# Optimization experiments

Measured on AMD Instinct MI355X. Metric: run time of the kernel, lower is better.

The kernel has to match this reference:

```python
import jax, jax.numpy as jnp
import numpy as np

B, L, C = 2, 1024, 512
H, P = 8, 4
D = C // H
LN_EPS = 1e-5


def setup_inputs() -> dict:
    key = jax.random.key(0)
    ks = jax.random.split(key, 12)
    s = 0.02
    inp = {
        "features": jax.random.normal(ks[0], (B, L, C), jnp.float32),
        "coords": jax.random.normal(ks[1], (B, L, 3), jnp.float32),
        # LayerNorm params
        "ln_g": jnp.ones((C,), jnp.float32),
        "ln_b": jnp.zeros((C,), jnp.float32),
        # scalar q/k/v projections (stored as [in, out])
        "wq": jax.random.normal(ks[2], (C, C), jnp.float32) * s,
        "bq": jnp.zeros((C,), jnp.float32),
        "wk": jax.random.normal(ks[3], (C, C), jnp.float32) * s,
        "bk": jnp.zeros((C,), jnp.float32),
        "wv": jax.random.normal(ks[4], (C, C), jnp.float32) * s,
        "bv": jnp.zeros((C,), jnp.float32),
        # point q/k/v projections: [C, H*P*3]
        "wqp": jax.random.normal(ks[5], (C, H * P * 3), jnp.float32) * s,
        "bqp": jnp.zeros((H * P * 3,), jnp.float32),
        "wkp": jax.random.normal(ks[6], (C, H * P * 3), jnp.float32) * s,
        "bkp": jnp.zeros((H * P * 3,), jnp.float32),
        "wvp": jax.random.normal(ks[7], (C, H * P * 3), jnp.float32) * s,
        "bvp": jnp.zeros((H * P * 3,), jnp.float32),
        # output projection
        "wo": jax.random.normal(ks[8], (C, C), jnp.float32) * s,
        "bo": jnp.zeros((C,), jnp.float32),
        # per-head point scale, init 1/sqrt(P)
        "pscale": jnp.full((H,), 1.0 / np.sqrt(P), jnp.float32),
    }
    return inp


def _layernorm(x, g, b):
    mu = jnp.mean(x, axis=-1, keepdims=True)
    var = jnp.mean((x - mu) ** 2, axis=-1, keepdims=True)
    return (x - mu) * jax.lax.rsqrt(var + LN_EPS) * g + b


def reference(features, coords, ln_g, ln_b, wq, bq, wk, bk, wv, bv,
              wqp, bqp, wkp, bkp, wvp, bvp, wo, bo, pscale):
    b, l, c = features.shape
    h = pscale.shape[0]
    d = c // h
    p = wqp.shape[1] // (h * 3)

    x = _layernorm(features, ln_g, ln_b)

    # scalar heads: [b,h,l,d]
    q_s = (x @ wq + bq).reshape(b, l, h, d).transpose(0, 2, 1, 3)
    k_s = (x @ wk + bk).reshape(b, l, h, d).transpose(0, 2, 1, 3)
    v_s = (x @ wv + bv).reshape(b, l, h, d).transpose(0, 2, 1, 3)

    # point heads: [b,h,l,p,3]
    q_p = (x @ wqp + bqp).reshape(b, l, h, p, 3).transpose(0, 2, 1, 3, 4)
    k_p = (x @ wkp + bkp).reshape(b, l, h, p, 3).transpose(0, 2, 1, 3, 4)

    # scalar logits
    logits_s = jnp.einsum('bhid,bhjd->bhij', q_s, k_s) * (d ** -0.5)

    # point-distance logits: sum_{p,k} ||q - k||^2 = |q|^2 + |k|^2 - 2 q.k
    # (avoids materializing the [b,h,l,l,p,3] difference tensor)
    dot = jnp.einsum('bhipk,bhjpk->bhij', q_p, k_p)
    qsq = jnp.sum(q_p * q_p, axis=(-1, -2))  # [b,h,l]
    ksq = jnp.sum(k_p * k_p, axis=(-1, -2))  # [b,h,l]
    pdist2 = qsq[..., :, None] + ksq[..., None, :] - 2.0 * dot  # [b,h,l,l]

    logits = logits_s - pdist2 * pscale[None, :, None, None]

    attn = jax.nn.softmax(logits, axis=-1)  # dropout is identity in eval

    out_s = jnp.einsum('bhij,bhjd->bhid', attn, v_s)
    out_s = out_s.transpose(0, 2, 1, 3).reshape(b, l, c)

    out = out_s @ wo + bo  # out_dropout is identity in eval
    return out
```

## Files before the change

kernel.cpp:

```cpp
#include <hip/hip_runtime.h>
#include <math.h>

#define BB 2
#define LL 1024
#define CCH 512
#define HH 8
#define LN_EPSF 1e-5f

typedef short s16x8 __attribute__((ext_vector_type(8)));
typedef float fx4 __attribute__((ext_vector_type(4)));


__device__ __forceinline__ unsigned short f2bf(float f) {
  unsigned u = __float_as_uint(f);
  unsigned r = (u + 0x7FFFu + ((u >> 16) & 1u)) >> 16;
  return (unsigned short)r;
}
__device__ __forceinline__ float bf2f(unsigned short h) {
  return __uint_as_float(((unsigned)h) << 16);
}
__device__ __forceinline__ s16x8 ldfrag(const unsigned short* p) {
  int4 t = *(const int4*)p;
  return *(s16x8*)&t;
}

template <int CTRL>
__device__ __forceinline__ float dpp_mov(float x) {
  return __int_as_float(
      __builtin_amdgcn_update_dpp(0, __float_as_int(x), CTRL, 0xF, 0xF, true));
}
__device__ __forceinline__ float red16_sum(float v) {
  v += dpp_mov<0x121>(v);
  v += dpp_mov<0x122>(v);
  v += dpp_mov<0x124>(v);
  v += dpp_mov<0x128>(v);
  return v;
}
__device__ __forceinline__ float red16_max(float v) {
  v = fmaxf(v, dpp_mov<0x121>(v));
  v = fmaxf(v, dpp_mov<0x122>(v));
  v = fmaxf(v, dpp_mov<0x124>(v));
  v = fmaxf(v, dpp_mov<0x128>(v));
  return v;
}
__device__ __forceinline__ float wave_sum(float v) {
  v = red16_sum(v);
  v += __shfl_xor(v, 16);
  v += __shfl_xor(v, 32);
  return v;
}

__global__ __launch_bounds__(256) void prep(
    const float* __restrict__ f, const float* __restrict__ g,
    const float* __restrict__ bta, unsigned short* __restrict__ xh,
    unsigned short* __restrict__ xl, const float* __restrict__ wq,
    const float* __restrict__ wk, const float* __restrict__ wv,
    const float* __restrict__ wo, const float* __restrict__ wqp,
    const float* __restrict__ wkp, unsigned short* __restrict__ wt_h) {
  __shared__ unsigned short lh[64][68];
  __shared__ float red[8];
  const int tid = threadIdx.x;
  if (blockIdx.x < 2048) {
    const int row = blockIdx.x;
    const int wave = tid >> 6, lane = tid & 63;
    const float* fr = f + (size_t)row * CCH;
    float2 v = *(const float2*)&fr[tid * 2];
    float s = wave_sum(v.x + v.y);
    if (lane == 0) red[wave] = s;
    __syncthreads();
    float mu = (red[0] + red[1] + red[2] + red[3]) * (1.0f / CCH);
    float dx = v.x - mu, dy = v.y - mu;
    float sq = wave_sum(dx * dx + dy * dy);
    if (lane == 0) red[4 + wave] = sq;
    __syncthreads();
    float var = (red[4] + red[5] + red[6] + red[7]) * (1.0f / CCH);
    float inv = 1.0f / sqrtf(var + LN_EPSF);
    float2 gg = *(const float2*)&g[tid * 2];
    float2 bb = *(const float2*)&bta[tid * 2];
    float ox = dx * inv * gg.x + bb.x;
    float oy = dy * inv * gg.y + bb.y;
    unsigned short h0 = f2bf(ox), h1 = f2bf(oy);
    ushort2 hv; hv.x = h0; hv.y = h1;
    ushort2 lv; lv.x = f2bf(ox - bf2f(h0)); lv.y = f2bf(oy - bf2f(h1));
    const int k0c = tid * 2;
    size_t addr = ((size_t)((row >> 4) * 16 + (k0c >> 5))) * 512 +
                  (((k0c >> 3) & 3) * 16 + (row & 15)) * 8 + (k0c & 7);
    *(ushort2*)&xh[addr] = hv;
    *(ushort2*)&xl[addr] = lv;
  } else {
    const int bx = blockIdx.x - 2048;
    const float* W;
    int Ncols, rowbase, kt, nt;
    if (bx < 256) {
      int mat = bx >> 6, t = bx & 63;
      kt = t >> 3; nt = t & 7; Ncols = 512;
      if (mat == 0) { W = wq; rowbase = 0; }
      else if (mat == 1) { W = wk; rowbase = 512; }
      else if (mat == 2) { W = wv; rowbase = 1024; }
      else { W = wo; rowbase = 1536; }
    } else {
      int r = bx - 256; int mat = r >> 4; int t = r & 15;
      kt = t >> 1; nt = t & 1; Ncols = 96;
      if (mat == 0) { W = wqp; rowbase = 2048; }
      else { W = wkp; rowbase = 2144; }
    }
    const int k0 = kt * 64, n0 = nt * 64;
    const int c = tid & 63;
#pragma unroll
    for (int ii = 0; ii < 16; ++ii) {
      int r = ii * 4 + (tid >> 6);
      float val = (n0 + c < Ncols) ? W[(size_t)(k0 + r) * Ncols + n0 + c] : 0.f;
      lh[r][c] = f2bf(val);
    }
    __syncthreads();
    const int base_nt = (rowbase >> 4) + (n0 >> 4);
    const int base_kt = (k0 >> 5);
#pragma unroll
    for (int cc = 0; cc < 2; ++cc) {
      int ch = cc * 256 + tid;
      int lane2 = ch & 63, ktl = (ch >> 6) & 1, ntl = ch >> 7;
      int l16c = lane2 & 15, quadc = lane2 >> 4;
      if (n0 + ntl * 16 < Ncols) {
        unsigned short th[8] __attribute__((aligned(16)));
#pragma unroll
        for (int jj = 0; jj < 8; ++jj)
          th[jj] = lh[ktl * 32 + quadc * 8 + jj][ntl * 16 + l16c];
        *(int4*)&wt_h[((size_t)((base_nt + ntl) * 16 + base_kt + ktl)) * 512 +
                      lane2 * 8] = *(int4*)th;
      }
    }
  }
}

template <int MF, int NF, int TERMS>
__device__ __forceinline__ void mfma_core_frag(
    const unsigned short* __restrict__ Ah, const unsigned short* __restrict__ Al,
    const unsigned short* __restrict__ Bt, int mt0, int ntbase, int nt0,
    int ntmax, int ks0, int ks1, fx4 acc[MF][NF]) {
  const int lane = threadIdx.x & 63;
  int bt[NF];
#pragma unroll
  for (int j = 0; j < NF; ++j) {
    int nt = nt0 + j;
    if (nt > ntmax) nt = ntmax;
    bt[j] = ntbase + nt;
  }
#pragma unroll
  for (int i = 0; i < MF; ++i)
#pragma unroll
    for (int j = 0; j < NF; ++j) acc[i][j] = (fx4){0.f, 0.f, 0.f, 0.f};
  for (int ks = ks0; ks < ks1; ++ks) {
    s16x8 ah[MF], al[MF], b[NF];
#pragma unroll
    for (int i = 0; i < MF; ++i) {
      size_t off = ((size_t)((mt0 + i) * 16 + ks)) * 512 + lane * 8;
      ah[i] = ldfrag(&Ah[off]);
      if (TERMS == 2) al[i] = ldfrag(&Al[off]);
    }
#pragma unroll
    for (int j = 0; j < NF; ++j)
      b[j] = ldfrag(&Bt[((size_t)(bt[j] * 16 + ks)) * 512 + lane * 8]);
#pragma unroll
    for (int i = 0; i < MF; ++i)
#pragma unroll
      for (int j = 0; j < NF; ++j) {
        acc[i][j] = __builtin_amdgcn_mfma_f32_16x16x32_bf16(ah[i], b[j], acc[i][j], 0, 0, 0);
        if (TERMS == 2)
          acc[i][j] = __builtin_amdgcn_mfma_f32_16x16x32_bf16(al[i], b[j], acc[i][j], 0, 0, 0);
      }
  }
}

__global__ __launch_bounds__(256, 4) void proj_mfma(
    const unsigned short* __restrict__ xh, const unsigned short* __restrict__ xl,
    const unsigned short* __restrict__ wt_h,
    const float* __restrict__ bq, const float* __restrict__ bk,
    const float* __restrict__ bv, const float* __restrict__ bqp,
    const float* __restrict__ bkp, const float* __restrict__ pscale,
    unsigned short* __restrict__ qt, unsigned short* __restrict__ kt_,
    unsigned short* __restrict__ vth) {
  __shared__ unsigned short vt_lds[64][72];
  const int bx = blockIdx.x;
  const int m0 = blockIdx.y * 64;
  const int tid = threadIdx.x;
  const int wave = __builtin_amdgcn_readfirstlane(tid >> 6);
  const int lane = tid & 63;
  const int quad = lane >> 4, l16 = lane & 15;
  const int mw = m0 + (wave & 1) * 32;
  const int mt0 = mw >> 4;

  if (bx < 16) {
    const bool isq = bx < 8;
    const float* bias = isq ? bq : bk;
    unsigned short* pdst = isq ? qt : kt_;
    const int n0 = (bx & 7) * 64;
    const int nw = n0 + (wave >> 1) * 32;
    fx4 acc[2][2];
    mfma_core_frag<2, 2, 1>(xh, xh, wt_h, mt0, isq ? 0 : 32, nw >> 4, 31, 0, 16, acc);
#pragma unroll
    for (int j = 0; j < 2; ++j) {
      int n = nw + j * 16 + l16;
      int h = n >> 6, d = n & 63;
      float bb = bias[n];
#pragma unroll
      for (int i = 0; i < 2; ++i)
#pragma unroll
        for (int reg = 0; reg < 4; ++reg) {
          int row = mw + i * 16 + quad * 4 + reg;
          int bi = row >> 10, l = row & 1023;
          int bh2 = bi * 8 + h;
          float val = (acc[i][j][reg] + bb) * 0.35355339059f;
          size_t tile = ((size_t)(bh2 * 64 + (l >> 4))) * 3 + (d >> 5);
          pdst[tile * 512 + (((d >> 3) & 3) * 16 + (l & 15)) * 8 + (d & 7)] = f2bf(val);
        }
    }
  } else if (bx < 24) {
    const int h = bx - 16;
    const int nw = h * 64 + (wave >> 1) * 32;
    fx4 acc[2][2];
    mfma_core_frag<2, 2, 2>(xh, xl, wt_h, mt0, 64, nw >> 4, 31, 0, 16, acc);
#pragma unroll
    for (int j = 0; j < 2; ++j) {
      int dl = (wave >> 1) * 32 + j * 16 + l16;
      float bb = bv[h * 64 + dl];
#pragma unroll
      for (int i = 0; i < 2; ++i)
#pragma unroll
        for (int reg = 0; reg < 4; ++reg) {
          int lm = (wave & 1) * 32 + i * 16 + quad * 4 + reg;
          vt_lds[lm][dl] = f2bf(acc[i][j][reg] + bb);
        }
    }
    __syncthreads();
    const int b = m0 >> 10, l0 = m0 & 1023;
    const int bh2 = b * 8 + h;
#pragma unroll
    for (int cc = 0; cc < 2; ++cc) {
      int ch = cc * 256 + tid;
      int lane2 = ch & 63, jt = (ch >> 6) & 1, ft = ch >> 7;
      int l16c = lane2 & 15, quadc = lane2 >> 4;
      unsigned short th[8] __attribute__((aligned(16)));
#pragma unroll
      for (int jj = 0; jj < 8; ++jj)
        th[jj] = vt_lds[jt * 32 + quadc * 8 + jj][ft * 16 + l16c];
      size_t tile = ((size_t)(bh2 * 4 + ft)) * 32 + (l0 >> 5) + jt;
      *(int4*)&vth[tile * 512 + lane2 * 8] = *(int4*)th;
    }
  } else {
    const bool isq = bx < 26;
    const float* bias = isq ? bqp : bkp;
    unsigned short* pdst = isq ? qt : kt_;
    const int n0 = (bx & 1) * 64;
    const int nw = n0 + (wave >> 1) * 32;
    fx4 acc[2][2];
    mfma_core_frag<2, 2, 1>(xh, xh, wt_h, mt0, isq ? 128 : 134, nw >> 4, 5, 0, 16, acc);
#pragma unroll
    for (int j = 0; j < 2; ++j) {
      int n = nw + j * 16 + l16;
      bool ok = n < 96;
      int nn = ok ? n : 0;
      int h = nn / 12, c = nn - h * 12;
      float sc = sqrtf(2.f * pscale[h]);
      float bb = bias[nn];
#pragma unroll
      for (int i = 0; i < 2; ++i)
#pragma unroll
        for (int reg = 0; reg < 4; ++reg) {
          int row = mw + i * 16 + quad * 4 + reg;
          int bi = row >> 10, l = row & 1023;
          int bh2 = bi * 8 + h;
          float val = (acc[i][j][reg] + bb) * sc;
          if (ok) {
            int kc = 64 + c;
            size_t tile = ((size_t)(bh2 * 64 + (l >> 4))) * 3 + 2;
            pdst[tile * 512 + (((kc >> 3) & 3) * 16 + (l & 15)) * 8 + (kc & 7)] =
                f2bf(val);
          }
        }
    }
  }
}

__global__ __launch_bounds__(256, 4) void out_proj_mfma(
    const unsigned short* __restrict__ oh,
    const unsigned short* __restrict__ wt_h, const float* __restrict__ bo,
    float* __restrict__ out) {
  const int tid = threadIdx.x;
  const int wave = __builtin_amdgcn_readfirstlane(tid >> 6);
  const int lane = tid & 63;
  const int quad = lane >> 4, l16 = lane & 15;
  const int mw = blockIdx.y * 64 + (wave & 1) * 32;
  const int nw = blockIdx.x * 64 + (wave >> 1) * 32;
  const int kz = blockIdx.z;
  fx4 acc[2][2];
  mfma_core_frag<2, 2, 1>(oh, oh, wt_h, mw >> 4, 96, nw >> 4, 31, kz * 4,
                          kz * 4 + 4, acc);
#pragma unroll
  for (int j = 0; j < 2; ++j) {
    int n = nw + j * 16 + l16;
    float bb = (kz == 0) ? bo[n] : 0.f;
#pragma unroll
    for (int i = 0; i < 2; ++i)
#pragma unroll
      for (int reg = 0; reg < 4; ++reg) {
        int row = mw + i * 16 + quad * 4 + reg;
        atomicAdd(&out[(size_t)row * 512 + n], acc[i][j][reg] + bb);
      }
  }
}

__global__ __launch_bounds__(256, 4) void ipa_attn_mfma(
    const unsigned short* __restrict__ qt, const unsigned short* __restrict__ kt_,
    const unsigned short* __restrict__ vth,
    float* __restrict__ po, float* __restrict__ pm, float* __restrict__ pl) {
  const int bid = blockIdx.x;
  const int low3 = bid & 7;
  const int slot = bid >> 3;
  const int qtile = slot & 31;
  const int t = slot >> 5;
  const int ksz = t & 1;
  const int bh = ((t >> 1) << 3) | low3;
  const int tid = threadIdx.x;
  const int wave = tid >> 6, lane = tid & 63;
  const int quad = lane >> 4, l16 = lane & 15;
  const int mstrip = wave & 1, khalf = wave >> 1;
  const int ibase = qtile * 32 + mstrip * 16;

  __shared__ unsigned short pb[4][16][32];
  __shared__ float obuf[4][16][64];
  __shared__ float mred[4][16], lred[4][16];
  __shared__ float qsl[4][16];

  s16x8 aq[3];
#pragma unroll
  for (int s = 0; s < 3; ++s)
    aq[s] = ldfrag(&qt[(((size_t)(bh * 64 + (ibase >> 4))) * 3 + s) * 512 + lane * 8]);

  {
    float qp = 0.f;
#pragma unroll
    for (int j = 0; j < 8; ++j) {
      float v = bf2f((unsigned short)aq[2][j]);
      qp += v * v;
    }
    qp += __shfl_xor(qp, 16);
    qp += __shfl_xor(qp, 32);
    qsl[wave][l16] = 0.5f * qp;
  }
  float qs_r[4];
#pragma unroll
  for (int reg = 0; reg < 4; ++reg) qs_r[reg] = qsl[wave][quad * 4 + reg];

  fx4 o[4];
#pragma unroll
  for (int f = 0; f < 4; ++f) o[f] = (fx4){0.f, 0.f, 0.f, 0.f};
  float m_r[4], l_r[4];
#pragma unroll
  for (int reg = 0; reg < 4; ++reg) { m_r[reg] = -INFINITY; l_r[reg] = 0.f; }

  for (int kt2 = ksz * 8; kt2 < ksz * 8 + 8; ++kt2) {
    const int j0 = kt2 * 64 + khalf * 32;
    s16x8 bk[2][3];
#pragma unroll
    for (int f = 0; f < 2; ++f)
#pragma unroll
      for (int s = 0; s < 3; ++s)
        bk[f][s] = ldfrag(
            &kt_[(((size_t)(bh * 64 + (j0 >> 4) + f)) * 3 + s) * 512 + lane * 8]);
    s16x8 bvh[4];
#pragma unroll
    for (int f = 0; f < 4; ++f)
      bvh[f] = ldfrag(
          &vth[(((size_t)(bh * 4 + f)) * 32 + (j0 >> 5)) * 512 + lane * 8]);

    float kp0 = 0.f, kp1 = 0.f;
#pragma unroll
    for (int j = 0; j < 8; ++j) {
      float v0 = bf2f((unsigned short)bk[0][2][j]);
      float v1 = bf2f((unsigned short)bk[1][2][j]);
      kp0 += v0 * v0;
      kp1 += v1 * v1;
    }
    kp0 += __shfl_xor(kp0, 16);
    kp0 += __shfl_xor(kp0, 32);
    kp1 += __shfl_xor(kp1, 16);
    kp1 += __shfl_xor(kp1, 32);
    float ks0 = 0.5f * kp0, ks1 = 0.5f * kp1;

    fx4 sa[2];
    sa[0] = (fx4){0.f, 0.f, 0.f, 0.f};
    sa[1] = (fx4){0.f, 0.f, 0.f, 0.f};
#pragma unroll
    for (int f = 0; f < 2; ++f)
#pragma unroll
      for (int s = 0; s < 3; ++s)
        sa[f] = __builtin_amdgcn_mfma_f32_16x16x32_bf16(aq[s], bk[f][s], sa[f], 0, 0, 0);

#pragma unroll
    for (int reg = 0; reg < 4; ++reg) {
      float z0 = sa[0][reg] - qs_r[reg] - ks0;
      float z1 = sa[1][reg] - qs_r[reg] - ks1;
      float mx = red16_max(fmaxf(z0, z1));
      float mnew = fmaxf(m_r[reg], mx);
      float p0 = __expf(z0 - mnew), p1 = __expf(z1 - mnew);
      float alpha = __expf(m_r[reg] - mnew);
      float psum = red16_sum(p0 + p1);
      l_r[reg] = l_r[reg] * alpha + psum;
      m_r[reg] = mnew;
      o[0][reg] *= alpha; o[1][reg] *= alpha; o[2][reg] *= alpha; o[3][reg] *= alpha;
      pb[wave][quad * 4 + reg][l16] = f2bf(p0);
      pb[wave][quad * 4 + reg][16 + l16] = f2bf(p1);
    }
    s16x8 ap = ldfrag(&pb[wave][l16][quad * 8]);
#pragma unroll
    for (int f = 0; f < 4; ++f)
      o[f] = __builtin_amdgcn_mfma_f32_16x16x32_bf16(ap, bvh[f], o[f], 0, 0, 0);
  }
  if (l16 == 0) {
#pragma unroll
    for (int reg = 0; reg < 4; ++reg) {
      mred[wave][quad * 4 + reg] = m_r[reg];
      lred[wave][quad * 4 + reg] = l_r[reg];
    }
  }
#pragma unroll
  for (int f = 0; f < 4; ++f)
#pragma unroll
    for (int reg = 0; reg < 4; ++reg)
      obuf[wave][quad * 4 + reg][f * 16 + l16] = o[f][reg];
  __syncthreads();
  if (khalf == 0) {
    const int pw = wave + 2;
    const size_t rbase = ((size_t)ksz * 16 + bh) * LL + ibase;
#pragma unroll
    for (int f = 0; f < 4; ++f)
#pragma unroll
      for (int reg = 0; reg < 4; ++reg) {
        int row = quad * 4 + reg;
        int d = f * 16 + l16;
        float m0v = mred[wave][row], m1v = mred[pw][row];
        float l0v = lred[wave][row], l1v = lred[pw][row];
        float M = fmaxf(m0v, m1v);
        float w0 = __expf(m0v - M), w1 = __expf(m1v - M);
        float Lv = l0v * w0 + l1v * w1;
        float val = obuf[wave][row][d] * w0 + obuf[pw][row][d] * w1;
        po[(rbase + row) * 64 + d] = val;
        if (f == 0 && l16 == 0) {
          pm[rbase + row] = M;
          pl[rbase + row] = Lv;
        }
      }
  }
}

__global__ __launch_bounds__(256) void merge_attn(const float* __restrict__ po,
                                                  const float* __restrict__ pm,
                                                  const float* __restrict__ pl,
                                                  unsigned short* __restrict__ oh) {
  const int r = blockIdx.x * 4 + (threadIdx.x >> 6);
  const int lane = threadIdx.x & 63;
  const size_t part = (size_t)16 * LL;
  float m0 = pm[r], m1 = pm[part + r];
  float l0 = pl[r], l1 = pl[part + r];
  float M = fmaxf(m0, m1);
  float w0 = __expf(m0 - M), w1 = __expf(m1 - M);
  float L = l0 * w0 + l1 * w1;
  float v = (po[(size_t)r * 64 + lane] * w0 + po[(part + r) * 64 + lane] * w1) / L;
  int bh = r >> 10, l = r & 1023;
  int b = bh >> 3, h = bh & 7;
  int m = b * LL + l;
  int kcol = h * 64 + lane;
  size_t tile = ((size_t)(m >> 4)) * 16 + (kcol >> 5);
  oh[tile * 512 + (((kcol >> 3) & 3) * 16 + (m & 15)) * 8 + (kcol & 7)] = f2bf(v);
}

extern "C" void kernel_launch(void* const* d_in, const int* in_sizes, int n_in,
                              void* d_out, int out_size, void* d_ws, size_t ws_size,
                              hipStream_t stream) {
  (void)in_sizes; (void)n_in; (void)out_size; (void)ws_size;
  const float* features = (const float*)d_in[0];
  const float* ln_g = (const float*)d_in[2];
  const float* ln_b = (const float*)d_in[3];
  const float* wq = (const float*)d_in[4];
  const float* bq = (const float*)d_in[5];
  const float* wk = (const float*)d_in[6];
  const float* bk = (const float*)d_in[7];
  const float* wv = (const float*)d_in[8];
  const float* bv = (const float*)d_in[9];
  const float* wqp = (const float*)d_in[10];
  const float* bqp = (const float*)d_in[11];
  const float* wkp = (const float*)d_in[12];
  const float* bkp = (const float*)d_in[13];
  const float* wo = (const float*)d_in[16];
  const float* bo = (const float*)d_in[17];
  const float* pscale = (const float*)d_in[18];
  float* out = (float*)d_out;

  char* cur = (char*)d_ws;
  const size_t NTOK = (size_t)BB * LL;
  unsigned short* xh = (unsigned short*)cur; cur += NTOK * CCH * 2;
  unsigned short* xl = (unsigned short*)cur; cur += NTOK * CCH * 2;
  unsigned short* wt_h = (unsigned short*)cur; cur += (size_t)2240 * 512 * 2;
  unsigned short* qt = (unsigned short*)cur; cur += (size_t)16 * LL * 96 * 2;
  unsigned short* kt_ = (unsigned short*)cur; cur += (size_t)16 * LL * 96 * 2;
  unsigned short* vth = (unsigned short*)cur; cur += (size_t)16 * 64 * LL * 2;
  unsigned short* oh = (unsigned short*)cur; cur += NTOK * CCH * 2;
  float* po = (float*)cur; cur += (size_t)2 * 16 * LL * 64 * 4;
  float* pm = (float*)cur; cur += (size_t)2 * 16 * LL * 4;
  float* pl = (float*)cur; cur += (size_t)2 * 16 * LL * 4;

  hipMemsetAsync(qt, 0, (size_t)2 * 16 * LL * 96 * 2, stream);
  hipMemsetAsync(out, 0, NTOK * CCH * 4, stream);

  prep<<<dim3(2048 + 288), 256, 0, stream>>>(features, ln_g, ln_b, xh, xl, wq, wk,
                                             wv, wo, wqp, wkp, wt_h);
  proj_mfma<<<dim3(28, 32), 256, 0, stream>>>(xh, xl, wt_h, bq, bk, bv, bqp, bkp,
                                              pscale, qt, kt_, vth);
  ipa_attn_mfma<<<dim3(1024), 256, 0, stream>>>(qt, kt_, vth, po, pm, pl);
  merge_attn<<<dim3(4096), 256, 0, stream>>>(po, pm, pl, oh);
  out_proj_mfma<<<dim3(8, 32, 4), 256, 0, stream>>>(oh, wt_h, bo, out);
}
```

Before: 165.8 us.

## Fuse split-K merge into attention kernel and fold memsets into prep

The attention kernel now uses 512-thread blocks with four key-quarter waves per query strip, so the full key range is processed in one block and the softmax partials are combined in shared memory before writing bf16 output directly. This removes the separate merge_attn kernel and the fp32 partial-output round trip through global memory. The two hipMemsetAsync calls are replaced by extra prep blocks that zero only the needed padding region of qt/kt and the output buffer, which cuts launches. In exchange there are half as many attention blocks, each with a larger shared-memory footprint, so occupancy and parallelism drop.

```diff
diff --git a/kernel.cpp b/kernel.cpp
--- a/kernel.cpp
+++ b/kernel.cpp
@@ -56,12 +56,15 @@
     unsigned short* __restrict__ xl, const float* __restrict__ wq,
     const float* __restrict__ wk, const float* __restrict__ wv,
     const float* __restrict__ wo, const float* __restrict__ wqp,
-    const float* __restrict__ wkp, unsigned short* __restrict__ wt_h) {
+    const float* __restrict__ wkp, unsigned short* __restrict__ wt_h,
+    unsigned short* __restrict__ qt, unsigned short* __restrict__ kt_,
+    float* __restrict__ out) {
   __shared__ unsigned short lh[64][68];
   __shared__ float red[8];
   const int tid = threadIdx.x;
-  if (blockIdx.x < 2048) {
-    const int row = blockIdx.x;
+  const int bxg = blockIdx.x;
+  if (bxg < 2048) {
+    const int row = bxg;
     const int wave = tid >> 6, lane = tid & 63;
     const float* fr = f + (size_t)row * CCH;
     float2 v = *(const float2*)&fr[tid * 2];
@@ -87,8 +90,8 @@
                   (((k0c >> 3) & 3) * 16 + (row & 15)) * 8 + (k0c & 7);
     *(ushort2*)&xh[addr] = hv;
     *(ushort2*)&xl[addr] = lv;
-  } else {
-    const int bx = blockIdx.x - 2048;
+  } else if (bxg < 2336) {
+    const int bx = bxg - 2048;
     const float* W;
     int Ncols, rowbase, kt, nt;
     if (bx < 256) {
@@ -129,6 +132,24 @@
                       lane2 * 8] = *(int4*)th;
       }
     }
+  } else if (bxg < 2400) {
+    const int vb2 = bxg - 2336;
+    const int4 zero = {0, 0, 0, 0};
+    for (int u = tid; u < 32 * 48; u += 256) {
+      int t = u / 48, off = (u - t * 48) * 8;
+      int gidx = vb2 * 32 + t;
+      unsigned short* dst = (gidx < 1024) ? qt : kt_;
+      int rem = gidx & 1023;
+      int bh = rem >> 6, lt = rem & 63;
+      size_t base = ((size_t)(bh * 64 + lt) * 3 + 2) * 512;
+      *(int4*)&dst[base + 128 + off] = zero;
+    }
+  } else {
+    const int vb3 = bxg - 2400;
+    const float4 zero = {0.f, 0.f, 0.f, 0.f};
+    float4* dst = (float4*)(out + (size_t)vb3 * 4096);
+#pragma unroll
+    for (int i = 0; i < 4; ++i) dst[i * 256 + tid] = zero;
   }
 }
 
@@ -309,27 +330,24 @@
   }
 }
 
-__global__ __launch_bounds__(256, 4) void ipa_attn_mfma(
+__global__ __launch_bounds__(512, 4) void ipa_attn_mfma(
     const unsigned short* __restrict__ qt, const unsigned short* __restrict__ kt_,
-    const unsigned short* __restrict__ vth,
-    float* __restrict__ po, float* __restrict__ pm, float* __restrict__ pl) {
+    const unsigned short* __restrict__ vth, unsigned short* __restrict__ oh) {
   const int bid = blockIdx.x;
   const int low3 = bid & 7;
   const int slot = bid >> 3;
   const int qtile = slot & 31;
-  const int t = slot >> 5;
-  const int ksz = t & 1;
-  const int bh = ((t >> 1) << 3) | low3;
+  const int bh = ((slot >> 5) << 3) | low3;
   const int tid = threadIdx.x;
   const int wave = tid >> 6, lane = tid & 63;
   const int quad = lane >> 4, l16 = lane & 15;
-  const int mstrip = wave & 1, khalf = wave >> 1;
+  const int mstrip = wave & 1, kq = wave >> 1;
   const int ibase = qtile * 32 + mstrip * 16;
 
-  __shared__ unsigned short pb[4][16][32];
-  __shared__ float obuf[4][16][64];
-  __shared__ float mred[4][16], lred[4][16];
-  __shared__ float qsl[4][16];
+  __shared__ unsigned short pb[8][16][32];
+  __shared__ float obuf[8][16][64];
+  __shared__ float mred[8][16], lred[8][16];
+  __shared__ float qsl[8][16];
 
   s16x8 aq[3];
 #pragma unroll
@@ -358,8 +376,9 @@
 #pragma unroll
   for (int reg = 0; reg < 4; ++reg) { m_r[reg] = -INFINITY; l_r[reg] = 0.f; }
 
-  for (int kt2 = ksz * 8; kt2 < ksz * 8 + 8; ++kt2) {
-    const int j0 = kt2 * 64 + khalf * 32;
+#pragma unroll 1
+  for (int c = 0; c < 8; ++c) {
+    const int j0 = kq * 256 + c * 32;
     s16x8 bk[2][3];
 #pragma unroll
     for (int f = 0; f < 2; ++f)
@@ -429,49 +448,32 @@
     for (int reg = 0; reg < 4; ++reg)
       obuf[wave][quad * 4 + reg][f * 16 + l16] = o[f][reg];
   __syncthreads();
-  if (khalf == 0) {
-    const int pw = wave + 2;
-    const size_t rbase = ((size_t)ksz * 16 + bh) * LL + ibase;
+  if (kq == 0) {
+    const int b = bh >> 3, h = bh & 7;
 #pragma unroll
     for (int f = 0; f < 4; ++f)
 #pragma unroll
       for (int reg = 0; reg < 4; ++reg) {
         int row = quad * 4 + reg;
         int d = f * 16 + l16;
-        float m0v = mred[wave][row], m1v = mred[pw][row];
-        float l0v = lred[wave][row], l1v = lred[pw][row];
-        float M = fmaxf(m0v, m1v);
-        float w0 = __expf(m0v - M), w1 = __expf(m1v - M);
-        float Lv = l0v * w0 + l1v * w1;
-        float val = obuf[wave][row][d] * w0 + obuf[pw][row][d] * w1;
-        po[(rbase + row) * 64 + d] = val;
-        if (f == 0 && l16 == 0) {
-          pm[rbase + row] = M;
-          pl[rbase + row] = Lv;
+        float M = -INFINITY;
+#pragma unroll
+        for (int p = 0; p < 4; ++p) M = fmaxf(M, mred[wave + p * 2][row]);
+        float L = 0.f, val = 0.f;
+#pragma unroll
+        for (int p = 0; p < 4; ++p) {
+          float w = __expf(mred[wave + p * 2][row] - M);
+          L += lred[wave + p * 2][row] * w;
+          val += obuf[wave + p * 2][row][d] * w;
         }
+        val /= L;
+        int m = b * LL + ibase + row;
+        int kcol = h * 64 + d;
+        size_t tile = ((size_t)(m >> 4)) * 16 + (kcol >> 5);
+        oh[tile * 512 + (((kcol >> 3) & 3) * 16 + (m & 15)) * 8 + (kcol & 7)] =
+            f2bf(val);
       }
   }
-}
-
-__global__ __launch_bounds__(256) void merge_attn(const float* __restrict__ po,
-                                                  const float* __restrict__ pm,
-                                                  const float* __restrict__ pl,
-                                                  unsigned short* __restrict__ oh) {
-  const int r = blockIdx.x * 4 + (threadIdx.x >> 6);
-  const int lane = threadIdx.x & 63;
-  const size_t part = (size_t)16 * LL;
-  float m0 = pm[r], m1 = pm[part + r];
-  float l0 = pl[r], l1 = pl[part + r];
-  float M = fmaxf(m0, m1);
-  float w0 = __expf(m0 - M), w1 = __expf(m1 - M);
-  float L = l0 * w0 + l1 * w1;
-  float v = (po[(size_t)r * 64 + lane] * w0 + po[(part + r) * 64 + lane] * w1) / L;
-  int bh = r >> 10, l = r & 1023;
-  int b = bh >> 3, h = bh & 7;
-  int m = b * LL + l;
-  int kcol = h * 64 + lane;
-  size_t tile = ((size_t)(m >> 4)) * 16 + (kcol >> 5);
-  oh[tile * 512 + (((kcol >> 3) & 3) * 16 + (m & 15)) * 8 + (kcol & 7)] = f2bf(v);
 }
 
 extern "C" void kernel_launch(void* const* d_in, const int* in_sizes, int n_in,
@@ -505,18 +507,11 @@
   unsigned short* kt_ = (unsigned short*)cur; cur += (size_t)16 * LL * 96 * 2;
   unsigned short* vth = (unsigned short*)cur; cur += (size_t)16 * 64 * LL * 2;
   unsigned short* oh = (unsigned short*)cur; cur += NTOK * CCH * 2;
-  float* po = (float*)cur; cur += (size_t)2 * 16 * LL * 64 * 4;
-  float* pm = (float*)cur; cur += (size_t)2 * 16 * LL * 4;
-  float* pl = (float*)cur; cur += (size_t)2 * 16 * LL * 4;
-
-  hipMemsetAsync(qt, 0, (size_t)2 * 16 * LL * 96 * 2, stream);
-  hipMemsetAsync(out, 0, NTOK * CCH * 4, stream);
-
-  prep<<<dim3(2048 + 288), 256, 0, stream>>>(features, ln_g, ln_b, xh, xl, wq, wk,
-                                             wv, wo, wqp, wkp, wt_h);
+
+  prep<<<dim3(2656), 256, 0, stream>>>(features, ln_g, ln_b, xh, xl, wq, wk, wv,
+                                       wo, wqp, wkp, wt_h, qt, kt_, out);
   proj_mfma<<<dim3(28, 32), 256, 0, stream>>>(xh, xl, wt_h, bq, bk, bv, bqp, bkp,
                                               pscale, qt, kt_, vth);
-  ipa_attn_mfma<<<dim3(1024), 256, 0, stream>>>(qt, kt_, vth, po, pm, pl);
-  merge_attn<<<dim3(4096), 256, 0, stream>>>(po, pm, pl, oh);
+  ipa_attn_mfma<<<dim3(512), 512, 0, stream>>>(qt, kt_, vth, oh);
   out_proj_mfma<<<dim3(8, 32, 4), 256, 0, stream>>>(oh, wt_h, bo, out);
 }
```

Result: faster. 155.5 us (-6.2%).
